# Optimization experiments

Measured on AMD Instinct MI355X. Metric: run time of the kernel, lower is better.

Reference implementation:

```python
import jax, jax.numpy as jnp
import numpy as np

B, C, NH, WS, NC = 8, 768, 12, 8, 1
HD = C // NH  # 64


def _window_partition(t, H, W):
    # t: [B, NH, H*W, HD] -> [B*nw, NH, WS*WS, HD]
    t = t.reshape(B, NH, H // WS, WS, W // WS, WS, HD)
    t = t.transpose(0, 2, 4, 1, 3, 5, 6)
    return t.reshape(-1, NH, WS * WS, HD)


def _window_reverse(t, H, W):
    # t: [B*nw, WS*WS, C] -> [B, H*W, C]
    t = t.reshape(B, H // WS, W // WS, WS, WS, C)
    t = t.transpose(0, 1, 3, 2, 4, 5)
    return t.reshape(B, H * W, C)


def setup_inputs() -> dict:
    key = jax.random.key(0)
    ks = jax.random.split(key, 8)
    H = W = 64
    N = NC + H * W
    x = jax.random.normal(ks[0], (B, N, C), jnp.float32)
    # per-token 0/1 mask broadcast over channels (matches mask@mask^T semantics)
    tok = (jax.random.uniform(ks[1], (B, H * W, 1)) > 0.2).astype(jnp.float32)
    mask = jnp.broadcast_to(tok, (B, H * W, C))
    global_mask = (jax.random.uniform(ks[2], (B, NH, NC, H * W)) > 0.5).astype(jnp.float32)
    s = 0.02
    qkv_w = jax.random.normal(ks[3], (C, 3 * C), jnp.float32) * s
    kv_global_w = jax.random.normal(ks[4], (C, 2 * C), jnp.float32) * s
    proj_w = jax.random.normal(ks[5], (C, C), jnp.float32) * s
    proj_b = jnp.zeros((C,), jnp.float32)
    return {"x": x, "mask": mask, "global_mask": global_mask, "qkv_w": qkv_w,
            "kv_global_w": kv_global_w, "proj_w": proj_w, "proj_b": proj_b,
            "H": H, "W": W}


def reference(x, mask, global_mask, qkv_w, kv_global_w, proj_w, proj_b, H, W):
    scale = HD ** -0.5
    HW = H * W
    NEG = -10000.0

    # qkv projection (no bias), split heads: [B, NH, N, HD]
    qkv = (x @ qkv_w).reshape(B, NC + HW, 3, NH, HD).transpose(2, 0, 3, 1, 4)
    q, k, v = qkv[0], qkv[1], qkv[2]
    m = mask.reshape(B, HW, NH, HD).transpose(0, 2, 1, 3)  # [B, NH, HW, HD]

    q_img, k_img, v_img = q[:, :, NC:], k[:, :, NC:], v[:, :, NC:]
    q_cls = q[:, :, :NC]

    # ---- local windowed attention ----
    qw = _window_partition(q_img, H, W)
    kw = _window_partition(k_img, H, W)
    vw = _window_partition(v_img, H, W)
    mw = _window_partition(m, H, W)
    am = (mw @ jnp.swapaxes(mw, -2, -1)) / HD          # [B*nw, NH, ws2, ws2]
    attn = (qw @ jnp.swapaxes(kw, -2, -1)) * scale
    attn = jnp.where(am == 0, NEG, attn)
    attn = jax.nn.softmax(attn, axis=-1)
    xl = (attn @ vw).transpose(0, 2, 1, 3).reshape(-1, WS * WS, C)
    x_img = _window_reverse(xl, H, W)                  # [B, HW, C]

    # ---- global aggregation (global tokens attend to image tokens) ----
    key_cov = jnp.sum(m, axis=-1) / HD                 # ones @ m^T / hd -> [B, NH, HW]
    am_g = key_cov[:, :, None, :] * global_mask        # [B, NH, NC, HW]
    attn_g = (q_cls @ jnp.swapaxes(k_img, -2, -1)) * scale
    attn_g = jnp.where(am_g == 0, NEG, attn_g)
    attn_g = jax.nn.softmax(attn_g, axis=-1)
    x_cls = (attn_g @ v_img).transpose(0, 2, 1, 3).reshape(B, NC, C)

    # kv_global projection of aggregated global tokens
    kv_g = (x_cls @ kv_global_w).reshape(B, NC, 2, NH, HD).transpose(2, 0, 3, 1, 4)
    k_cls, v_cls = kv_g[0], kv_g[1]                    # [B, NH, NC, HD]

    # ---- global broadcast (image tokens attend to global tokens) ----
    am_b = (jnp.sum(m, axis=-1) / HD)[..., None]       # m @ ones^T / hd -> [B, NH, HW, 1]
    am_b = jnp.broadcast_to(am_b, (B, NH, HW, NC))
    attn_b = (q_img @ jnp.swapaxes(k_cls, -2, -1)) * scale
    attn_b = jnp.where(am_b == 0, NEG, attn_b)
    attn_b = jax.nn.softmax(attn_b, axis=-1)
    xb = (attn_b @ v_cls).transpose(0, 2, 1, 3).reshape(B, HW, C)

    x_img = x_img + xb
    out = jnp.concatenate([x_cls, x_img], axis=1) @ proj_w + proj_b
    return out
```

## Files before the change

### kernel.cpp

```cpp
#include <hip/hip_runtime.h>

#define B_    8
#define C_    768
#define NH_   12
#define HW_   4096
#define NTOK  4097
#define MTOT  32776
#define NEGV  (-10000.0f)
#define NSPLIT 16

typedef __bf16 bf16x8 __attribute__((ext_vector_type(8)));
typedef float  f32x4  __attribute__((ext_vector_type(4)));
typedef unsigned short us8 __attribute__((ext_vector_type(8)));

#define GLB(p) ((const __attribute__((address_space(1))) void*)(p))
#define LDS(p) ((__attribute__((address_space(3))) void*)(p))

__device__ __forceinline__ float us2f(unsigned short u) {
    unsigned int v = ((unsigned int)u) << 16;
    float f; __builtin_memcpy(&f, &v, 4);
    return f;
}
__device__ __forceinline__ unsigned short f2us(float f) {
    unsigned int v; __builtin_memcpy(&v, &f, 4);
    v += 0x7FFFu + ((v >> 16) & 1u);
    return (unsigned short)(v >> 16);
}

__global__ __launch_bounds__(256) void detect_dtype(
    const unsigned int* __restrict__ xw, int* __restrict__ flag)
{
    __shared__ int s[256];
    int t = threadIdx.x, cnt = 0;
    for (int i = t; i < 4096; i += 256) {
        unsigned e = (xw[i] >> 23) & 0xFFu;
        cnt += (e >= 64u && e <= 191u) ? 1 : 0;
    }
    s[t] = cnt; __syncthreads();
    for (int k = 128; k > 0; k >>= 1) { if (t < k) s[t] += s[t + k]; __syncthreads(); }
    if (t == 0) *flag = (s[0] > 2048) ? 1 : 0;
}

__global__ __launch_bounds__(256) void transpose_w(
    const unsigned short* __restrict__ s16, const float* __restrict__ s32,
    const int* __restrict__ flagp, unsigned short* __restrict__ dst,
    int Kd, int Nd)
{
    int o = blockIdx.x * 256 + threadIdx.x;
    if (o >= Kd * Nd) return;
    int n = o / Kd, k = o % Kd;
    dst[o] = (*flagp) ? f2us(s32[(size_t)k * Nd + n]) : s16[(size_t)k * Nd + n];
}

__global__ __launch_bounds__(256) void gemm_bt(
    const unsigned short* __restrict__ A16, const float* __restrict__ A32,
    const int* __restrict__ aflagp,
    const unsigned short* __restrict__ BT,
    const unsigned short* __restrict__ bias16, const float* __restrict__ bias32,
    const int* __restrict__ bflagp,
    void* __restrict__ Cout, const int* __restrict__ oflagp,
    int M, int Nd, int K, long arow0)
{
    __shared__ __align__(16) unsigned short As[128 * 32];
    __shared__ __align__(16) unsigned short Bs[128 * 32];

    const int fa = aflagp ? *aflagp : 0;
    const int fb = bflagp ? *bflagp : 0;
    const int fo = oflagp ? *oflagp : 0;

    const int t    = threadIdx.x;
    const int m0   = blockIdx.y * 128;
    const int n0   = blockIdx.x * 128;
    const int wave = t >> 6;
    const int lane = t & 63;
    const int wm   = (wave >> 1) * 64;
    const int wn   = (wave & 1) * 64;
    const int frow = lane & 15;
    const int koff = (lane >> 4) * 8;

    f32x4 acc[4][4];
#pragma unroll
    for (int i = 0; i < 4; ++i)
#pragma unroll
        for (int j = 0; j < 4; ++j) acc[i][j] = (f32x4)0.0f;

    const int sr = t >> 2;
    const int sc = (t & 3) * 8;

    int ga0 = m0 + sr;       if (ga0 >= M)  ga0 = M - 1;
    int ga1 = m0 + sr + 64;  if (ga1 >= M)  ga1 = M - 1;
    int gb0 = n0 + sr;       if (gb0 >= Nd) gb0 = Nd - 1;
    int gb1 = n0 + sr + 64;  if (gb1 >= Nd) gb1 = Nd - 1;

    const unsigned short* a0p = A16 + (size_t)(arow0 + ga0) * K + sc;
    const unsigned short* a1p = A16 + (size_t)(arow0 + ga1) * K + sc;
    const float*          a0f = A32 + (size_t)(arow0 + ga0) * K + sc;
    const float*          a1f = A32 + (size_t)(arow0 + ga1) * K + sc;
    const unsigned short* b0p = BT + (size_t)gb0 * K + sc;
    const unsigned short* b1p = BT + (size_t)gb1 * K + sc;

    unsigned short* asd = &As[t * 8];
    unsigned short* bsd = &Bs[t * 8];

    for (int k0 = 0; k0 < K; k0 += 32) {
        if (fa) {
            unsigned short tmp[8];
#pragma unroll
            for (int e = 0; e < 8; ++e) tmp[e] = f2us(a0f[k0 + e]);
            *reinterpret_cast<us8*>(&As[sr * 32 + sc]) = *reinterpret_cast<us8*>(tmp);
#pragma unroll
            for (int e = 0; e < 8; ++e) tmp[e] = f2us(a1f[k0 + e]);
            *reinterpret_cast<us8*>(&As[(sr + 64) * 32 + sc]) = *reinterpret_cast<us8*>(tmp);
        } else {
            __builtin_amdgcn_global_load_lds(GLB(a0p + k0), LDS(asd),        16, 0, 0);
            __builtin_amdgcn_global_load_lds(GLB(a1p + k0), LDS(asd + 2048), 16, 0, 0);
        }
        __builtin_amdgcn_global_load_lds(GLB(b0p + k0), LDS(bsd),        16, 0, 0);
        __builtin_amdgcn_global_load_lds(GLB(b1p + k0), LDS(bsd + 2048), 16, 0, 0);
        __syncthreads();

        bf16x8 af[4], bfr[4];
#pragma unroll
        for (int i = 0; i < 4; ++i)
            af[i] = *reinterpret_cast<const bf16x8*>(&As[(wm + i * 16 + frow) * 32 + koff]);
#pragma unroll
        for (int j = 0; j < 4; ++j)
            bfr[j] = *reinterpret_cast<const bf16x8*>(&Bs[(wn + j * 16 + frow) * 32 + koff]);
#pragma unroll
        for (int i = 0; i < 4; ++i)
#pragma unroll
            for (int j = 0; j < 4; ++j)
                acc[i][j] = __builtin_amdgcn_mfma_f32_16x16x32_bf16(af[i], bfr[j], acc[i][j], 0, 0, 0);
        __syncthreads();
    }

    const int crow = (lane >> 4) * 4;
    const int ccol = lane & 15;
    unsigned short* C16 = (unsigned short*)Cout;
    float*          C32 = (float*)Cout;
#pragma unroll
    for (int i = 0; i < 4; ++i)
#pragma unroll
        for (int j = 0; j < 4; ++j) {
            int gn = n0 + wn + j * 16 + ccol;
            float bv = 0.0f;
            if (bias16) bv = fb ? bias32[gn] : us2f(bias16[gn]);
#pragma unroll
            for (int r = 0; r < 4; ++r) {
                int gm = m0 + wm + i * 16 + crow + r;
                if (gm < M) {
                    float v = acc[i][j][r] + bv;
                    if (fo) C32[(size_t)gm * Nd + gn] = v;
                    else    C16[(size_t)gm * Nd + gn] = f2us(v);
                }
            }
        }
}

#define LSTR 40

__global__ __launch_bounds__(256) void gemm_univ(
    const unsigned short* __restrict__ A16, const float* __restrict__ A32,
    const int* __restrict__ aflagp,
    const unsigned short* __restrict__ B16, const float* __restrict__ B32,
    const int* __restrict__ bflagp, int btmode,
    const unsigned short* __restrict__ bias16, const float* __restrict__ bias32,
    void* __restrict__ Cout, const int* __restrict__ oflagp,
    int M, int Nd, int K, long arow0)
{
    __shared__ __align__(16) unsigned short As[128 * LSTR];
    __shared__ __align__(16) unsigned short Bs[128 * LSTR];

    const int fa = aflagp ? *aflagp : 0;
    const int fb = bflagp ? *bflagp : 0;
    const int fo = oflagp ? *oflagp : 0;

    const int t    = threadIdx.x;
    const int m0   = blockIdx.y * 128;
    const int n0   = blockIdx.x * 128;
    const int wave = t >> 6;
    const int lane = t & 63;
    const int wm   = (wave >> 1) * 64;
    const int wn   = (wave & 1) * 64;
    const int frow = lane & 15;
    const int koff = (lane >> 4) * 8;

    f32x4 acc[4][4];
#pragma unroll
    for (int i = 0; i < 4; ++i)
#pragma unroll
        for (int j = 0; j < 4; ++j) acc[i][j] = (f32x4)0.0f;

    const int sr = t >> 2;
    const int sc = (t & 3) * 8;

    for (int k0 = 0; k0 < K; k0 += 32) {
#pragma unroll
        for (int it = 0; it < 2; ++it) {
            int r = sr + it * 64;
            int gl = m0 + r; if (gl >= M) gl = M - 1;
            size_t grow = (size_t)(arow0 + gl);
            if (fa) {
                const float* p = &A32[grow * K + k0 + sc];
                unsigned short tmp[8];
#pragma unroll
                for (int e = 0; e < 8; ++e) tmp[e] = f2us(p[e]);
                *reinterpret_cast<us8*>(&As[r * LSTR + sc]) = *reinterpret_cast<us8*>(tmp);
            } else {
                *reinterpret_cast<bf16x8*>(&As[r * LSTR + sc]) =
                    *reinterpret_cast<const bf16x8*>(&A16[grow * K + k0 + sc]);
            }
        }
        if (btmode == 0) {
#pragma unroll
            for (int it = 0; it < 2; ++it) {
                int r = sr + it * 64;
                int gn = n0 + r; if (gn >= Nd) gn = Nd - 1;
                *reinterpret_cast<bf16x8*>(&Bs[r * LSTR + sc]) =
                    *reinterpret_cast<const bf16x8*>(&B16[(size_t)gn * K + k0 + sc]);
            }
        } else {
            const int kr = t >> 3;
            const int nc = (t & 7) * 16;
            if (fb) {
                const float* p = &B32[(size_t)(k0 + kr) * Nd + n0 + nc];
#pragma unroll
                for (int e = 0; e < 16; ++e) Bs[(nc + e) * LSTR + kr] = f2us(p[e]);
            } else {
                const unsigned short* p = &B16[(size_t)(k0 + kr) * Nd + n0 + nc];
#pragma unroll
                for (int e = 0; e < 16; ++e) Bs[(nc + e) * LSTR + kr] = p[e];
            }
        }
        __syncthreads();

        bf16x8 af[4], bfr[4];
#pragma unroll
        for (int i = 0; i < 4; ++i)
            af[i] = *reinterpret_cast<const bf16x8*>(&As[(wm + i * 16 + frow) * LSTR + koff]);
#pragma unroll
        for (int j = 0; j < 4; ++j)
            bfr[j] = *reinterpret_cast<const bf16x8*>(&Bs[(wn + j * 16 + frow) * LSTR + koff]);
#pragma unroll
        for (int i = 0; i < 4; ++i)
#pragma unroll
            for (int j = 0; j < 4; ++j)
                acc[i][j] = __builtin_amdgcn_mfma_f32_16x16x32_bf16(af[i], bfr[j], acc[i][j], 0, 0, 0);
        __syncthreads();
    }

    const int crow = (lane >> 4) * 4;
    const int ccol = lane & 15;
    unsigned short* C16 = (unsigned short*)Cout;
    float*          C32 = (float*)Cout;
#pragma unroll
    for (int i = 0; i < 4; ++i)
#pragma unroll
        for (int j = 0; j < 4; ++j) {
            int gn = n0 + wn + j * 16 + ccol;
            float bv = 0.0f;
            if (bias16) bv = fb ? bias32[gn] : us2f(bias16[gn]);
#pragma unroll
            for (int r = 0; r < 4; ++r) {
                int gm = m0 + wm + i * 16 + crow + r;
                if (gm < M) {
                    float v = acc[i][j][r] + bv;
                    if (fo) C32[(size_t)gm * Nd + gn] = v;
                    else    C16[(size_t)gm * Nd + gn] = f2us(v);
                }
            }
        }
}

#define AST 72
#define SST 65

__global__ __launch_bounds__(256) void win_attn(
    const unsigned short* __restrict__ qkv2,
    const unsigned short* __restrict__ m16, const float* __restrict__ m32,
    const int* __restrict__ flagp,
    unsigned short* __restrict__ xcat, int b0)
{
    __shared__ __align__(16) unsigned short qs[64 * AST];
    __shared__ __align__(16) unsigned short ks[64 * AST];
    __shared__ __align__(16) unsigned short vsT[64 * AST];
    __shared__ float S[64 * SST];
    __shared__ float tok[64];

    const int w  = blockIdx.x;
    const int h  = blockIdx.y;
    const int bb = blockIdx.z;
    const int b  = b0 + bb;
    const int hb = w >> 3, wb = w & 7;
    const int t  = threadIdx.x;
    const int f  = *flagp;
    const unsigned short* qkvb = qkv2 + (size_t)bb * NTOK * 2304;

#define POS(i) ((hb * 8 + ((i) >> 3)) * 64 + wb * 8 + ((i) & 7))

#pragma unroll
    for (int it = 0; it < 2; ++it) {
        int i = (t >> 3) + it * 32;
        int d = (t & 7) * 8;
        size_t row = (size_t)(1 + POS(i)) * 2304;
        bf16x8 qv = *reinterpret_cast<const bf16x8*>(&qkvb[row + 0    + h * 64 + d]);
        bf16x8 kv = *reinterpret_cast<const bf16x8*>(&qkvb[row + 768  + h * 64 + d]);
        us8    vv = *reinterpret_cast<const us8*>  (&qkvb[row + 1536 + h * 64 + d]);
        *reinterpret_cast<bf16x8*>(&qs[i * AST + d]) = qv;
        *reinterpret_cast<bf16x8*>(&ks[i * AST + d]) = kv;
#pragma unroll
        for (int e = 0; e < 8; ++e) vsT[(d + e) * AST + i] = vv[e];
    }
    if (t < 64) {
        size_t mi = ((size_t)b * HW_ + POS(t)) * C_;
        tok[t] = f ? m32[mi] : us2f(m16[mi]);
    }
    __syncthreads();

    const int wave = t >> 6;
    const int lane = t & 63;
    const int wm   = (wave >> 1) * 32;
    const int wn   = (wave & 1) * 32;
    const int frow = lane & 15;
    const int koff = (lane >> 4) * 8;
    const int crow = (lane >> 4) * 4;
    const int ccol = lane & 15;

    {
        f32x4 acc[2][2];
#pragma unroll
        for (int i = 0; i < 2; ++i)
#pragma unroll
            for (int j = 0; j < 2; ++j) acc[i][j] = (f32x4)0.0f;
#pragma unroll
        for (int kk = 0; kk < 64; kk += 32) {
            bf16x8 af[2], bfr[2];
#pragma unroll
            for (int i = 0; i < 2; ++i)
                af[i] = *reinterpret_cast<const bf16x8*>(&qs[(wm + i * 16 + frow) * AST + kk + koff]);
#pragma unroll
            for (int j = 0; j < 2; ++j)
                bfr[j] = *reinterpret_cast<const bf16x8*>(&ks[(wn + j * 16 + frow) * AST + kk + koff]);
#pragma unroll
            for (int i = 0; i < 2; ++i)
#pragma unroll
                for (int j = 0; j < 2; ++j)
                    acc[i][j] = __builtin_amdgcn_mfma_f32_16x16x32_bf16(af[i], bfr[j], acc[i][j], 0, 0, 0);
        }
#pragma unroll
        for (int i = 0; i < 2; ++i)
#pragma unroll
            for (int j = 0; j < 2; ++j)
#pragma unroll
                for (int r = 0; r < 4; ++r)
                    S[(wm + i * 16 + crow + r) * SST + wn + j * 16 + ccol] = acc[i][j][r];
    }
    __syncthreads();

    {
        const int r = t >> 2;
        const int q = t & 3;
        const float tr = tok[r];
        float sv[16];
        float mx = -1e30f;
#pragma unroll
        for (int e = 0; e < 16; ++e) {
            int c = q * 16 + e;
            float s = S[r * SST + c] * 0.125f;
            if (tr * tok[c] == 0.0f) s = NEGV;
            sv[e] = s;
            mx = fmaxf(mx, s);
        }
        mx = fmaxf(mx, __shfl_xor(mx, 1));
        mx = fmaxf(mx, __shfl_xor(mx, 2));
        float sum = 0.f;
#pragma unroll
        for (int e = 0; e < 16; ++e) { sv[e] = __expf(sv[e] - mx); sum += sv[e]; }
        sum += __shfl_xor(sum, 1);
        sum += __shfl_xor(sum, 2);
        const float inv = 1.0f / sum;
        unsigned short* ps = qs;
        us8 o0, o1;
#pragma unroll
        for (int e = 0; e < 8; ++e) { o0[e] = f2us(sv[e] * inv); o1[e] = f2us(sv[8 + e] * inv); }
        *reinterpret_cast<us8*>(&ps[r * AST + q * 16])     = o0;
        *reinterpret_cast<us8*>(&ps[r * AST + q * 16 + 8]) = o1;
    }
    __syncthreads();

    {
        const unsigned short* ps = qs;
        f32x4 acc[2][2];
#pragma unroll
        for (int i = 0; i < 2; ++i)
#pragma unroll
            for (int j = 0; j < 2; ++j) acc[i][j] = (f32x4)0.0f;
#pragma unroll
        for (int kk = 0; kk < 64; kk += 32) {
            bf16x8 af[2], bfr[2];
#pragma unroll
            for (int i = 0; i < 2; ++i)
                af[i] = *reinterpret_cast<const bf16x8*>(&ps[(wm + i * 16 + frow) * AST + kk + koff]);
#pragma unroll
            for (int j = 0; j < 2; ++j)
                bfr[j] = *reinterpret_cast<const bf16x8*>(&vsT[(wn + j * 16 + frow) * AST + kk + koff]);
#pragma unroll
            for (int i = 0; i < 2; ++i)
#pragma unroll
                for (int j = 0; j < 2; ++j)
                    acc[i][j] = __builtin_amdgcn_mfma_f32_16x16x32_bf16(af[i], bfr[j], acc[i][j], 0, 0, 0);
        }
#pragma unroll
        for (int i = 0; i < 2; ++i)
#pragma unroll
            for (int j = 0; j < 2; ++j)
#pragma unroll
                for (int r = 0; r < 4; ++r) {
                    int qrow = wm + i * 16 + crow + r;
                    int dcol = wn + j * 16 + ccol;
                    xcat[(size_t)(b * NTOK + 1 + POS(qrow)) * C_ + h * 64 + dcol] =
                        f2us(acc[i][j][r]);
                }
    }
#undef POS
}

__global__ __launch_bounds__(256) void cls_part(
    const unsigned short* __restrict__ qkv2,
    const unsigned short* __restrict__ m16, const float* __restrict__ m32,
    const unsigned short* __restrict__ g16, const float* __restrict__ g32,
    const int* __restrict__ flagp,
    float* __restrict__ part,
    int b0)
{
    __shared__ float q[64];
    __shared__ float e[256];
    __shared__ float red[256];
    __shared__ float osum[4][64];
    __shared__ float Mv, Sv;

    const int h  = blockIdx.x;
    const int sp = blockIdx.y;
    const int bb = blockIdx.z;
    const int b  = b0 + bb;
    const int t  = threadIdx.x;
    const int f  = *flagp;
    const unsigned short* qkvb = qkv2 + (size_t)bb * NTOK * 2304;

    if (t < 64) q[t] = us2f(qkvb[h * 64 + t]);
    __syncthreads();

    const int j = sp * 256 + t;
    const unsigned short* krow = &qkvb[(size_t)(1 + j) * 2304 + 768 + h * 64];
    float s = 0.f;
#pragma unroll
    for (int dd = 0; dd < 8; ++dd) {
        us8 kv8 = *reinterpret_cast<const us8*>(&krow[dd * 8]);
#pragma unroll
        for (int ee = 0; ee < 8; ++ee) s += q[dd * 8 + ee] * us2f(kv8[ee]);
    }
    s *= 0.125f;
    {
        size_t mi = ((size_t)b * HW_ + j) * C_;
        size_t gi = ((size_t)b * NH_ + h) * HW_ + j;
        float tokj = f ? m32[mi] : us2f(m16[mi]);
        float gmj  = f ? g32[gi] : us2f(g16[gi]);
        if (tokj * gmj == 0.0f) s = NEGV;
    }

    red[t] = s; __syncthreads();
    for (int k2 = 128; k2 > 0; k2 >>= 1) { if (t < k2) red[t] = fmaxf(red[t], red[t + k2]); __syncthreads(); }
    const float m = red[0]; __syncthreads();

    float ev = __expf(s - m);
    e[t] = ev; red[t] = ev; __syncthreads();
    for (int k2 = 128; k2 > 0; k2 >>= 1) { if (t < k2) red[t] += red[t + k2]; __syncthreads(); }
    if (t == 0) { Mv = m; Sv = red[0]; }

    const int wv = t >> 6, l = t & 63;
    float accv = 0.f;
    const unsigned short* vbase =
        &qkvb[(size_t)(1 + sp * 256 + wv * 64) * 2304 + 1536 + h * 64 + l];
    for (int kk = 0; kk < 64; ++kk)
        accv += e[wv * 64 + kk] * us2f(vbase[(size_t)kk * 2304]);
    osum[wv][l] = accv;
    __syncthreads();

    const size_t pi = ((size_t)(b * NH_ + h) * NSPLIT + sp) * 68;
    if (t < 64)
        part[pi + t] = osum[0][t] + osum[1][t] + osum[2][t] + osum[3][t];
    if (t == 64 + 0) part[pi + 64] = Mv;
    if (t == 64 + 1) part[pi + 65] = Sv;
}

__global__ __launch_bounds__(64) void cls_reduce(
    const float* __restrict__ part, unsigned short* __restrict__ xcat)
{
    const int h = blockIdx.x, b = blockIdx.y, t = threadIdx.x;
    const float* pb = &part[((size_t)(b * NH_ + h) * NSPLIT) * 68];
    float gm = -1e30f;
    for (int i = 0; i < NSPLIT; ++i) gm = fmaxf(gm, pb[i * 68 + 64]);
    float S = 0.f, acc = 0.f;
    for (int i = 0; i < NSPLIT; ++i) {
        float w = __expf(pb[i * 68 + 64] - gm);
        S   += pb[i * 68 + 65] * w;
        acc += pb[i * 68 + t]  * w;
    }
    xcat[(size_t)(b * NTOK) * C_ + h * 64 + t] = f2us(acc / S);
}

__global__ __launch_bounds__(256) void add_vcls(
    const unsigned short* __restrict__ xcat, unsigned short* __restrict__ xcatc,
    const unsigned short* __restrict__ kv16, const float* __restrict__ kv32,
    const int* __restrict__ flagp)
{
    __shared__ float xr[768];
    __shared__ float psum[4][64];
    __shared__ float vc[64];

    const int blk = blockIdx.x;
    const int rsp = blockIdx.y;
    const int b   = blk / 12;
    const int c0  = (blk % 12) * 64;
    const int t   = threadIdx.x;
    const int f   = *flagp;

    for (int it = 0; it < 3; ++it) {
        int k = t + it * 256;
        xr[k] = us2f(xcat[(size_t)(b * NTOK) * C_ + k]);
    }
    __syncthreads();

    const int cc = t & 63, kq = t >> 6;
    float p = 0.f;
    for (int k = kq * 192; k < kq * 192 + 192; ++k) {
        size_t wi = (size_t)k * 1536 + 768 + c0 + cc;
        p += xr[k] * (f ? kv32[wi] : us2f(kv16[wi]));
    }
    psum[kq][cc] = p;
    __syncthreads();
    if (t < 64) vc[t] = psum[0][t] + psum[1][t] + psum[2][t] + psum[3][t];
    __syncthreads();

    const int ch8  = (t & 7) * 8;
    const int rsub = t >> 3;
    for (int it = 0; it < 32; ++it) {
        int row = rsp * 1024 + it * 32 + rsub;
        size_t off = (size_t)(b * NTOK + 1 + row) * C_ + c0 + ch8;
        us8 vv = *reinterpret_cast<const us8*>(&xcat[off]);
#pragma unroll
        for (int e2 = 0; e2 < 8; ++e2)
            vv[e2] = f2us(us2f(vv[e2]) + vc[ch8 + e2]);
        *reinterpret_cast<us8*>(&xcatc[off]) = vv;
    }
    if (rsp == 0 && t < 64)
        xcatc[(size_t)(b * NTOK) * C_ + c0 + t] = xcat[(size_t)(b * NTOK) * C_ + c0 + t];
}

extern "C" void kernel_launch(void* const* d_in, const int* in_sizes, int n_in,
                              void* d_out, int out_size, void* d_ws, size_t ws_size,
                              hipStream_t stream)
{
    const unsigned short* x16  = (const unsigned short*)d_in[0];
    const float*          x32  = (const float*)d_in[0];
    const unsigned short* m16  = (const unsigned short*)d_in[1];
    const float*          m32  = (const float*)d_in[1];
    const unsigned short* g16  = (const unsigned short*)d_in[2];
    const float*          g32  = (const float*)d_in[2];
    const unsigned short* qw16 = (const unsigned short*)d_in[3];
    const float*          qw32 = (const float*)d_in[3];
    const unsigned short* kv16 = (const unsigned short*)d_in[4];
    const float*          kv32 = (const float*)d_in[4];
    const unsigned short* pw16 = (const unsigned short*)d_in[5];
    const float*          pw32 = (const float*)d_in[5];
    const unsigned short* pb16 = (const unsigned short*)d_in[6];
    const float*          pb32 = (const float*)d_in[6];

    char* ws = (char*)d_ws;
    int*            flag   = (int*)ws;
    unsigned short* qkv_2b = (unsigned short*)(ws + 128);
    unsigned short* qkv_wT = (unsigned short*)(ws + 37758080);
    float*          part   = (float*)(ws + 41297024);
    unsigned short* xcatc  = (unsigned short*)(ws + 128);
    unsigned short* pwT    = (unsigned short*)(ws + 50344064);
    unsigned short* xcat   = (unsigned short*)d_out;

    const bool fastproj = (ws_size >= (size_t)51523712);

    detect_dtype<<<1, 256, 0, stream>>>((const unsigned int*)d_in[0], flag);
    transpose_w<<<(2304 * 768 + 255) / 256, 256, 0, stream>>>(
        qw16, qw32, flag, qkv_wT, 768, 2304);
    if (fastproj)
        transpose_w<<<(768 * 768 + 255) / 256, 256, 0, stream>>>(
            pw16, pw32, flag, pwT, 768, 768);

    for (int b0 = 0; b0 < B_; b0 += 2) {
        gemm_bt<<<dim3(18, 65), 256, 0, stream>>>(
            x16, x32, flag, qkv_wT,
            nullptr, nullptr, nullptr,
            qkv_2b, nullptr,
            2 * NTOK, 2304, 768, (long)b0 * NTOK);
        win_attn<<<dim3(64, 12, 2), 256, 0, stream>>>(qkv_2b, m16, m32, flag, xcat, b0);
        cls_part<<<dim3(12, NSPLIT, 2), 256, 0, stream>>>(
            qkv_2b, m16, m32, g16, g32, flag, part, b0);
    }

    cls_reduce<<<dim3(12, 8), 64, 0, stream>>>(part, xcat);
    add_vcls<<<dim3(96, 4), 256, 0, stream>>>(xcat, xcatc, kv16, kv32, flag);

    if (fastproj) {
        gemm_bt<<<dim3(6, 257), 256, 0, stream>>>(
            xcatc, nullptr, nullptr, pwT,
            pb16, pb32, flag,
            d_out, flag,
            MTOT, 768, 768, 0);
    } else {
        gemm_univ<<<dim3(6, 257), 256, 0, stream>>>(
            xcatc, nullptr, nullptr, pw16, pw32, flag, 1,
            pb16, pb32, d_out, flag,
            MTOT, 768, 768, 0);
    }
}
```

Before: 799.4 us.

## Deepen GEMM K-tile with XOR-swizzled LDS and batch all images per launch

The bf16 GEMM now stages 64-wide K tiles instead of 32, using an XOR swizzle on the LDS column chunks to avoid bank conflicts. This halves the barrier count per K and doubles the MFMA work between syncs. The host side gains a fused path: when the workspace is large enough, QKV projection, window attention and class-token partials run once over all 8 images instead of four 2-image chunks. That cuts launch count and gives larger grids, at the cost of a much larger workspace and double the LDS per GEMM block, which may reduce occupancy.

```diff
diff --git a/kernel.cpp b/kernel.cpp
--- a/kernel.cpp
+++ b/kernel.cpp
@@ -61,8 +61,8 @@
     void* __restrict__ Cout, const int* __restrict__ oflagp,
     int M, int Nd, int K, long arow0)
 {
-    __shared__ __align__(16) unsigned short As[128 * 32];
-    __shared__ __align__(16) unsigned short Bs[128 * 32];
+    __shared__ __align__(16) unsigned short As[128 * 64];
+    __shared__ __align__(16) unsigned short Bs[128 * 64];
 
     const int fa = aflagp ? *aflagp : 0;
     const int fb = bflagp ? *bflagp : 0;
@@ -76,7 +76,7 @@
     const int wm   = (wave >> 1) * 64;
     const int wn   = (wave & 1) * 64;
     const int frow = lane & 15;
-    const int koff = (lane >> 4) * 8;
+    const int lsl  = lane >> 4;
 
     f32x4 acc[4][4];
 #pragma unroll
@@ -84,53 +84,61 @@
 #pragma unroll
         for (int j = 0; j < 4; ++j) acc[i][j] = (f32x4)0.0f;
 
-    const int sr = t >> 2;
-    const int sc = (t & 3) * 8;
-
-    int ga0 = m0 + sr;       if (ga0 >= M)  ga0 = M - 1;
-    int ga1 = m0 + sr + 64;  if (ga1 >= M)  ga1 = M - 1;
-    int gb0 = n0 + sr;       if (gb0 >= Nd) gb0 = Nd - 1;
-    int gb1 = n0 + sr + 64;  if (gb1 >= Nd) gb1 = Nd - 1;
-
-    const unsigned short* a0p = A16 + (size_t)(arow0 + ga0) * K + sc;
-    const unsigned short* a1p = A16 + (size_t)(arow0 + ga1) * K + sc;
-    const float*          a0f = A32 + (size_t)(arow0 + ga0) * K + sc;
-    const float*          a1f = A32 + (size_t)(arow0 + ga1) * K + sc;
-    const unsigned short* b0p = BT + (size_t)gb0 * K + sc;
-    const unsigned short* b1p = BT + (size_t)gb1 * K + sc;
-
-    unsigned short* asd = &As[t * 8];
-    unsigned short* bsd = &Bs[t * 8];
-
-    for (int k0 = 0; k0 < K; k0 += 32) {
+    const int tr   = t >> 3;
+    const int srcc = (((t & 7) ^ (tr & 7)) * 8);
+
+    const float* aF[4];
+    const unsigned short* aP[4];
+    const unsigned short* bP[4];
+#pragma unroll
+    for (int it = 0; it < 4; ++it) {
+        int ga = m0 + tr + it * 32; if (ga >= M)  ga = M - 1;
+        int gb = n0 + tr + it * 32; if (gb >= Nd) gb = Nd - 1;
+        aP[it] = A16 + (size_t)(arow0 + ga) * K + srcc;
+        aF[it] = A32 + (size_t)(arow0 + ga) * K + srcc;
+        bP[it] = BT  + (size_t)gb * K + srcc;
+    }
+
+    for (int k0 = 0; k0 < K; k0 += 64) {
         if (fa) {
-            unsigned short tmp[8];
-#pragma unroll
-            for (int e = 0; e < 8; ++e) tmp[e] = f2us(a0f[k0 + e]);
-            *reinterpret_cast<us8*>(&As[sr * 32 + sc]) = *reinterpret_cast<us8*>(tmp);
-#pragma unroll
-            for (int e = 0; e < 8; ++e) tmp[e] = f2us(a1f[k0 + e]);
-            *reinterpret_cast<us8*>(&As[(sr + 64) * 32 + sc]) = *reinterpret_cast<us8*>(tmp);
+#pragma unroll
+            for (int it = 0; it < 4; ++it) {
+                unsigned short tmp[8];
+                const float* p = aF[it] + k0;
+#pragma unroll
+                for (int e = 0; e < 8; ++e) tmp[e] = f2us(p[e]);
+                *reinterpret_cast<us8*>(&As[it * 2048 + t * 8]) = *reinterpret_cast<us8*>(tmp);
+            }
         } else {
-            __builtin_amdgcn_global_load_lds(GLB(a0p + k0), LDS(asd),        16, 0, 0);
-            __builtin_amdgcn_global_load_lds(GLB(a1p + k0), LDS(asd + 2048), 16, 0, 0);
-        }
-        __builtin_amdgcn_global_load_lds(GLB(b0p + k0), LDS(bsd),        16, 0, 0);
-        __builtin_amdgcn_global_load_lds(GLB(b1p + k0), LDS(bsd + 2048), 16, 0, 0);
+#pragma unroll
+            for (int it = 0; it < 4; ++it)
+                __builtin_amdgcn_global_load_lds(GLB(aP[it] + k0), LDS(&As[it * 2048 + t * 8]), 16, 0, 0);
+        }
+#pragma unroll
+        for (int it = 0; it < 4; ++it)
+            __builtin_amdgcn_global_load_lds(GLB(bP[it] + k0), LDS(&Bs[it * 2048 + t * 8]), 16, 0, 0);
         __syncthreads();
 
-        bf16x8 af[4], bfr[4];
-#pragma unroll
-        for (int i = 0; i < 4; ++i)
-            af[i] = *reinterpret_cast<const bf16x8*>(&As[(wm + i * 16 + frow) * 32 + koff]);
-#pragma unroll
-        for (int j = 0; j < 4; ++j)
-            bfr[j] = *reinterpret_cast<const bf16x8*>(&Bs[(wn + j * 16 + frow) * 32 + koff]);
-#pragma unroll
-        for (int i = 0; i < 4; ++i)
-#pragma unroll
-            for (int j = 0; j < 4; ++j)
-                acc[i][j] = __builtin_amdgcn_mfma_f32_16x16x32_bf16(af[i], bfr[j], acc[i][j], 0, 0, 0);
+#pragma unroll
+        for (int kk = 0; kk < 64; kk += 32) {
+            const int ksl = (kk >> 3) + lsl;
+            bf16x8 af[4], bfr[4];
+#pragma unroll
+            for (int i = 0; i < 4; ++i) {
+                int ra = wm + i * 16 + frow;
+                af[i] = *reinterpret_cast<const bf16x8*>(&As[ra * 64 + ((ksl ^ (ra & 7)) << 3)]);
+            }
+#pragma unroll
+            for (int j = 0; j < 4; ++j) {
+                int rb = wn + j * 16 + frow;
+                bfr[j] = *reinterpret_cast<const bf16x8*>(&Bs[rb * 64 + ((ksl ^ (rb & 7)) << 3)]);
+            }
+#pragma unroll
+            for (int i = 0; i < 4; ++i)
+#pragma unroll
+                for (int j = 0; j < 4; ++j)
+                    acc[i][j] = __builtin_amdgcn_mfma_f32_16x16x32_bf16(af[i], bfr[j], acc[i][j], 0, 0, 0);
+        }
         __syncthreads();
     }
 
@@ -577,17 +585,51 @@
     const float*          pb32 = (const float*)d_in[6];
 
     char* ws = (char*)d_ws;
-    int*            flag   = (int*)ws;
+    int*            flag  = (int*)ws;
+    unsigned short* xcatc = (unsigned short*)(ws + 128);
+    unsigned short* xcat  = (unsigned short*)d_out;
+
+    const bool fused = (ws_size >= (size_t)156168320);
+
+    detect_dtype<<<1, 256, 0, stream>>>((const unsigned int*)d_in[0], flag);
+
+    if (fused) {
+        unsigned short* qkv_full = (unsigned short*)(ws + 128);
+        unsigned short* qkv_wT   = (unsigned short*)(ws + 151031936);
+        float*          part     = (float*)(ws + 154570880);
+        unsigned short* pwT      = (unsigned short*)(ws + 154988672);
+
+        transpose_w<<<(2304 * 768 + 255) / 256, 256, 0, stream>>>(
+            qw16, qw32, flag, qkv_wT, 768, 2304);
+        transpose_w<<<(768 * 768 + 255) / 256, 256, 0, stream>>>(
+            pw16, pw32, flag, pwT, 768, 768);
+
+        gemm_bt<<<dim3(18, 257), 256, 0, stream>>>(
+            x16, x32, flag, qkv_wT,
+            nullptr, nullptr, nullptr,
+            qkv_full, nullptr,
+            MTOT, 2304, 768, 0);
+        win_attn<<<dim3(64, 12, 8), 256, 0, stream>>>(qkv_full, m16, m32, flag, xcat, 0);
+        cls_part<<<dim3(12, NSPLIT, 8), 256, 0, stream>>>(
+            qkv_full, m16, m32, g16, g32, flag, part, 0);
+
+        cls_reduce<<<dim3(12, 8), 64, 0, stream>>>(part, xcat);
+        add_vcls<<<dim3(96, 4), 256, 0, stream>>>(xcat, xcatc, kv16, kv32, flag);
+
+        gemm_bt<<<dim3(6, 257), 256, 0, stream>>>(
+            xcatc, nullptr, nullptr, pwT,
+            pb16, pb32, flag,
+            d_out, flag,
+            MTOT, 768, 768, 0);
+        return;
+    }
+
     unsigned short* qkv_2b = (unsigned short*)(ws + 128);
     unsigned short* qkv_wT = (unsigned short*)(ws + 37758080);
     float*          part   = (float*)(ws + 41297024);
-    unsigned short* xcatc  = (unsigned short*)(ws + 128);
     unsigned short* pwT    = (unsigned short*)(ws + 50344064);
-    unsigned short* xcat   = (unsigned short*)d_out;
-
     const bool fastproj = (ws_size >= (size_t)51523712);
 
-    detect_dtype<<<1, 256, 0, stream>>>((const unsigned int*)d_in[0], flag);
     transpose_w<<<(2304 * 768 + 255) / 256, 256, 0, stream>>>(
         qw16, qw32, flag, qkv_wT, 768, 2304);
     if (fastproj)
```

After: 769.8 us. 1.04x faster.
